# Performance work log

Hardware: AMD Instinct MI355X
Metric: run time of the kernel (lower is better)

The kernel has to match this reference:

```python
import jax, jax.numpy as jnp
import numpy as np

NUM_HEAD = 16


def setup_inputs() -> dict:
    key = jax.random.key(0)
    ks = jax.random.split(key, 4)
    B, C, D = 2, 2048, 1024
    hidden_states = jax.random.normal(ks[0], (B, C, D), dtype=jnp.float32)
    attention_mask = jnp.zeros((B, 1, C, C), dtype=jnp.float32)
    Wqkv = jax.random.normal(ks[1], (D, 3 * D), dtype=jnp.float32) * (D ** -0.5)
    bqkv = jnp.zeros((3 * D,), dtype=jnp.float32)
    Wo = jax.random.normal(ks[2], (D, D), dtype=jnp.float32) * (D ** -0.5)
    bo = jnp.zeros((D,), dtype=jnp.float32)
    return {"hidden_states": hidden_states, "attention_mask": attention_mask,
            "Wqkv": Wqkv, "bqkv": bqkv, "Wo": Wo, "bo": bo}


def reference(hidden_states, attention_mask, Wqkv, bqkv, Wo, bo):
    B, C, D = hidden_states.shape
    H = NUM_HEAD
    hd = D // H
    scaling = hd ** -0.5

    qkv = hidden_states @ Wqkv + bqkv                      # [B, C, 3D]
    q, k, v = jnp.split(qkv, 3, axis=-1)
    # [B, C, H, hd] -> [B, H, C, hd]
    q = q.reshape(B, C, H, hd).transpose(0, 2, 1, 3)
    k = k.reshape(B, C, H, hd).transpose(0, 2, 1, 3)
    v = v.reshape(B, C, H, hd).transpose(0, 2, 1, 3)

    scores = jnp.einsum("bhqd,bhkd->bhqk", q, k) * scaling  # [B, H, C, C]
    causal = jnp.tril(jnp.ones((C, C), dtype=bool))[None, None]
    mask = jnp.where(causal, attention_mask, -jnp.inf)      # [B, 1, C, C]
    probs = jax.nn.softmax(scores + mask, axis=-1)
    out = jnp.einsum("bhqk,bhkd->bhqd", probs, v)           # [B, H, C, hd]
    out = out.transpose(0, 2, 1, 3).reshape(B, C, D)
    return out @ Wo + bo
```

## Files before the change

### kernel.cpp

```cpp
#include <hip/hip_runtime.h>
#include <hip/hip_bf16.h>
#include <cstdint>
#include <cstddef>

typedef __attribute__((ext_vector_type(8))) short short8;
typedef __attribute__((ext_vector_type(4))) float f32x4;
typedef __attribute__((ext_vector_type(16))) float f32x16;
typedef unsigned short u16;
typedef unsigned int u32;

#define B_ 2
#define C_ 2048
#define D_ 1024
#define H_ 16
#define HD_ 64

static __device__ __forceinline__ u16 f2b(float f) {
  u32 x = __builtin_bit_cast(u32, f);
  x += 0x7FFFu + ((x >> 16) & 1u);
  return (u16)(x >> 16);
}
static __device__ __forceinline__ float b2f(u16 v) {
  return __builtin_bit_cast(float, (u32)v << 16);
}

static __device__ void tconv_body(const float* __restrict__ in, u16* __restrict__ out,
                                  int R, int Cc, int bx, int by, int t,
                                  float (*tile)[65]) {
  const int tC = bx * 64, tR = by * 64;
  const int r0 = t >> 4;
  const int c0 = (t & 15) * 4;
#pragma unroll
  for (int ii = 0; ii < 4; ++ii) {
    int r = ii * 16 + r0;
    float4 v = *reinterpret_cast<const float4*>(&in[(size_t)(tR + r) * Cc + tC + c0]);
    tile[r][c0] = v.x; tile[r][c0 + 1] = v.y; tile[r][c0 + 2] = v.z; tile[r][c0 + 3] = v.w;
  }
  __syncthreads();
#pragma unroll
  for (int ii = 0; ii < 4; ++ii) {
    int c = ii * 16 + r0;
    ushort4 o;
    o.x = f2b(tile[c0 + 0][c]);
    o.y = f2b(tile[c0 + 1][c]);
    o.z = f2b(tile[c0 + 2][c]);
    o.w = f2b(tile[c0 + 3][c]);
    *reinterpret_cast<ushort4*>(&out[(size_t)(tC + c) * R + tR + c0]) = o;
  }
}

__global__ __launch_bounds__(256) void k_prep(
    const float* __restrict__ hs, u16* __restrict__ hsb,
    const float* __restrict__ Wqkv, u16* __restrict__ Wqkvt,
    const float* __restrict__ Wo, u16* __restrict__ Wot,
    const float* __restrict__ mask, u32* __restrict__ flags)
{
  __shared__ float tile[64][65];
  __shared__ int sh[4];
  const int bid = blockIdx.x;
  const int t = threadIdx.x;
  if (bid < 2048) {
    int i = (bid * 256 + t) * 4;
    const int n = 4096 * 1024;
    const int stride = 2048 * 256 * 4;
    for (; i < n; i += stride) {
      float4 v = *reinterpret_cast<const float4*>(hs + i);
      ushort4 o;
      o.x = f2b(v.x); o.y = f2b(v.y); o.z = f2b(v.z); o.w = f2b(v.w);
      *reinterpret_cast<ushort4*>(hsb + i) = o;
    }
  } else if (bid < 2816) {
    const int r = bid - 2048;
    tconv_body(Wqkv, Wqkvt, 1024, 3072, r % 48, r / 48, t, tile);
  } else if (bid < 3072) {
    const int r = bid - 2816;
    tconv_body(Wo, Wot, 1024, 1024, r % 16, r / 16, t, tile);
  } else {
    const int mb = bid - 3072;
    const int kt = mb & 31, qs = (mb >> 5) & 31, b = mb >> 10;
    const float* base = mask + ((size_t)b * C_ + qs * 64) * C_ + kt * 64;
    const int row = t >> 2, c0 = (t & 3) * 16;
    int any = 0;
#pragma unroll
    for (int i = 0; i < 4; ++i) {
      float4 v = *reinterpret_cast<const float4*>(base + (size_t)row * C_ + c0 + i * 4);
      any |= (v.x != 0.f) | (v.y != 0.f) | (v.z != 0.f) | (v.w != 0.f);
    }
    const unsigned long long bal = __ballot(any);
    if ((t & 63) == 0) sh[t >> 6] = (bal != 0ull);
    __syncthreads();
    if (t == 0) flags[mb] = (u32)(sh[0] | sh[1] | sh[2] | sh[3]);
  }
}

#define GLL16(gptr, lptr) __builtin_amdgcn_global_load_lds( \
    (const __attribute__((address_space(1))) u32*)(gptr),   \
    (__attribute__((address_space(3))) u32*)(lptr), 16, 0, 0)

template<int EPI, int BM>
__global__ __launch_bounds__(256) void k_gemm(
    const u16* __restrict__ A, const u16* __restrict__ Bt,
    int M, int N, int K, const float* __restrict__ bias,
    u16* __restrict__ Cq, u16* __restrict__ Ck, u16* __restrict__ Cv,
    float* __restrict__ Cf)
{
  constexpr int WCW = (BM == 128) ? 64 : 32;
  constexpr int NF = WCW / 16;
  __shared__ __align__(16) u16 As[BM * 64];
  __shared__ __align__(16) u16 Bs[128 * 64];
  const int t = threadIdx.x;
  const int l = t & 63, w = t >> 6;
  const int wr = (BM == 128) ? (w >> 1) : 0;
  const int wc = (BM == 128) ? (w & 1) : w;
  const int lr = l & 15, lg = l >> 4;
  const int swk = lr & 7;
  const int m0 = blockIdx.y * BM, n0 = blockIdx.x * 128;
  f32x4 acc[4][NF] = {};

  for (int k0 = 0; k0 < K; k0 += 64) {
#pragma unroll
    for (int s = 0; s < BM / 32; ++s) {
      const int u = s * 256 + t;
      const int row = u >> 3, slot = (u & 7) ^ (row & 7);
      GLL16(A + (size_t)(m0 + row) * K + k0 + (slot << 3), As + (u << 3));
    }
#pragma unroll
    for (int s = 0; s < 4; ++s) {
      const int u = s * 256 + t;
      const int row = u >> 3, slot = (u & 7) ^ (row & 7);
      GLL16(Bt + (size_t)(n0 + row) * K + k0 + (slot << 3), Bs + (u << 3));
    }
    __syncthreads();
    short8 af[2][4], bfr[2][NF];
#pragma unroll
    for (int s = 0; s < 2; ++s) {
#pragma unroll
      for (int m = 0; m < 4; ++m)
        af[s][m] = *reinterpret_cast<const short8*>(
            &As[((wr * 64 + m * 16 + lr) << 6) + (((s * 4 + lg) ^ swk) << 3)]);
#pragma unroll
      for (int n = 0; n < NF; ++n)
        bfr[s][n] = *reinterpret_cast<const short8*>(
            &Bs[((wc * WCW + n * 16 + lr) << 6) + (((s * 4 + lg) ^ swk) << 3)]);
    }
#pragma unroll
    for (int s = 0; s < 2; ++s)
#pragma unroll
      for (int m = 0; m < 4; ++m)
#pragma unroll
        for (int n = 0; n < NF; ++n)
          acc[m][n] = __builtin_amdgcn_mfma_f32_16x16x32_bf16(af[s][m], bfr[s][n], acc[m][n], 0, 0, 0);
    __syncthreads();
  }

#pragma unroll
  for (int m = 0; m < 4; ++m) {
    const int mg = m0 + wr * 64 + m * 16 + lg * 4;
    const int bq = mg >> 11, c0 = mg & 2047;
#pragma unroll
    for (int n = 0; n < NF; ++n) {
      const int ng = n0 + wc * WCW + n * 16 + lr;
      const float bia = bias[ng];
      if (EPI == 0) {
        const int reg = ng >> 10, d = ng & 1023, h = d >> 6, e = d & 63;
        if (reg == 2) {
          u16* vp = Cv + (((size_t)(bq * H_ + h) * HD_ + e) << 11) + c0;
#pragma unroll
          for (int j = 0; j < 4; ++j) vp[j] = f2b(acc[m][n][j] + bia);
        } else {
          u16* dst = (reg == 0) ? Cq : Ck;
#pragma unroll
          for (int j = 0; j < 4; ++j)
            dst[(((size_t)(bq * H_ + h) * C_ + c0 + j) << 6) + e] = f2b(acc[m][n][j] + bia);
        }
      } else {
#pragma unroll
        for (int j = 0; j < 4; ++j)
          Cf[(size_t)(mg + j) * N + ng] = acc[m][n][j] + bia;
      }
    }
  }
}

static __device__ __forceinline__ void stage_kv(
    const u16* __restrict__ Kbh, const u16* __restrict__ Vbh,
    u16* Kd, u16* Vd, int kt, int t)
{
#pragma unroll
  for (int ch = 0; ch < 2; ++ch) {
    const int u = ch * 256 + t;
    const int row = u >> 3, slot = (u & 7) ^ (row & 7);
    GLL16(Kbh + (((size_t)(kt * 64 + row)) << 6) + (slot << 3), Kd + (u << 3));
    GLL16(Vbh + (((size_t)row) << 11) + kt * 64 + (slot << 3), Vd + (u << 3));
  }
}

__global__ __launch_bounds__(256) void k_attn(
    const u16* __restrict__ Q, const u16* __restrict__ Kb, const u16* __restrict__ Vt,
    const float* __restrict__ mask, const u32* __restrict__ flags,
    u16* __restrict__ O, u16* __restrict__ Opart, float2* __restrict__ ml)
{
  __shared__ __align__(16) u16 Kl[2][64 * 64];
  __shared__ __align__(16) u16 Vl[2][64 * 64];
  __shared__ __align__(16) u16 Sc[4][2304];
  const int bid = blockIdx.x;
  const int bh = bid & 31;
  const int sidx = 23 - (bid >> 5);
  int qt, seg, nseg;
  if (sidx < 8) { qt = sidx; seg = 0; nseg = 1; }
  else          { const int u = sidx - 8; qt = 8 + (u >> 1); seg = u & 1; nseg = 2; }
  const int ntiles = 2 * qt + 2;
  const int kt0 = seg * 16;
  const int kt1 = seg ? ntiles : ((ntiles < 16) ? ntiles : 16);
  const int slot = ((bh << 3) + (qt - 8)) * 2 + seg;

  const int b = bh >> 4, h = bh & 15;
  const int t = threadIdx.x;
  const int l = t & 63, w = t >> 6;
  const int q = l & 31, hi = l >> 5;
  const int q7 = q & 7;

  const u16* Kbh = Kb + (size_t)bh * (C_ * HD_);
  const u16* Vbh = Vt + (size_t)bh * (HD_ * C_);
  char* Swb = reinterpret_cast<char*>(Sc[w]);

  const int q0w = qt * 128 + w * 32;
  const int qg = q0w + q;
  const int qmaxw = q0w + 31;

  short8 aq[4];
  {
    const u16* qp = Q + ((size_t)bh * C_ + qg) * HD_ + hi * 8;
#pragma unroll
    for (int kh = 0; kh < 4; ++kh) {
      short8 v = *reinterpret_cast<const short8*>(qp + kh * 16);
#pragma unroll
      for (int i = 0; i < 8; ++i) {
        const float f = b2f((u16)v[i]) * 0.125f;
        v[i] = (short)f2b(f);
      }
      aq[kh] = v;
    }
  }

  f32x16 oa0 = {}, oa1 = {};
  float mrun = -INFINITY, srun = 0.f;
  const float* mrow = mask + ((size_t)b * C_ + qg) * C_;
  const u32* fb = flags + (size_t)(b * 32 + (q0w >> 6)) * 32;

  stage_kv(Kbh, Vbh, Kl[0], Vl[0], kt0, t);

#pragma unroll 1
  for (int kt = kt0; kt < kt1; ++kt) {
    const int cur = kt & 1;
    __syncthreads();
    if (kt + 1 < kt1) stage_kv(Kbh, Vbh, Kl[cur ^ 1], Vl[cur ^ 1], kt + 1, t);
    if (kt * 64 > qmaxw) continue;

    const char* Kc = reinterpret_cast<const char*>(Kl[cur]);
    const char* Vc = reinterpret_cast<const char*>(Vl[cur]);

    f32x16 p0 = {}, p1 = {};
#pragma unroll
    for (int kh = 0; kh < 4; ++kh) {
      const int sl = ((2 * kh + hi) ^ q7) << 4;
      const short8 k0 = *reinterpret_cast<const short8*>(Kc + q * 128 + sl);
      const short8 k1 = *reinterpret_cast<const short8*>(Kc + (32 + q) * 128 + sl);
      p0 = __builtin_amdgcn_mfma_f32_32x32x16_bf16(k0, aq[kh], p0, 0, 0, 0);
      p1 = __builtin_amdgcn_mfma_f32_32x32x16_bf16(k1, aq[kh], p1, 0, 0, 0);
    }

    if (fb[kt]) {
      const float* mp = mrow + kt * 64 + 4 * hi;
#pragma unroll
      for (int g = 0; g < 4; ++g) {
        const float4 m0 = *reinterpret_cast<const float4*>(mp + 8 * g);
        const float4 m1 = *reinterpret_cast<const float4*>(mp + 32 + 8 * g);
        p0[4*g+0] += m0.x; p0[4*g+1] += m0.y; p0[4*g+2] += m0.z; p0[4*g+3] += m0.w;
        p1[4*g+0] += m1.x; p1[4*g+1] += m1.y; p1[4*g+2] += m1.z; p1[4*g+3] += m1.w;
      }
    }
    if (kt * 64 + 63 > q0w) {
#pragma unroll
      for (int r = 0; r < 16; ++r) {
        const int kl = kt * 64 + (r & 3) + 8 * (r >> 2) + 4 * hi;
        if (kl > qg) p0[r] = -INFINITY;
        if (kl + 32 > qg) p1[r] = -INFINITY;
      }
    }

    float pm = -INFINITY;
#pragma unroll
    for (int r = 0; r < 16; ++r) pm = fmaxf(pm, fmaxf(p0[r], p1[r]));
    pm = fmaxf(pm, __shfl_xor(pm, 32));
    const float mn = fmaxf(fmaxf(mrun, pm), -1e30f);
    const float rs = __expf(mrun - mn);
    float sum = 0.f;
#pragma unroll
    for (int r = 0; r < 16; ++r) {
      p0[r] = __expf(p0[r] - mn); sum += p0[r];
      p1[r] = __expf(p1[r] - mn); sum += p1[r];
    }
    sum += __shfl_xor(sum, 32);
    srun = srun * rs + sum;
    mrun = mn;
    oa0 *= rs; oa1 *= rs;

#pragma unroll
    for (int g = 0; g < 4; ++g) {
#pragma unroll
      for (int m = 0; m < 2; ++m) {
        u32 w0, w1;
        asm("v_cvt_pk_bf16_f32 %0, %1, %2" : "=v"(w0) : "v"(p0[4*g+2*m]), "v"(p0[4*g+2*m+1]));
        asm("v_cvt_pk_bf16_f32 %0, %1, %2" : "=v"(w1) : "v"(p1[4*g+2*m]), "v"(p1[4*g+2*m+1]));
        *reinterpret_cast<u32*>(Swb + q * 128 + ((g ^ q7) << 4) + 8 * hi + 4 * m) = w0;
        *reinterpret_cast<u32*>(Swb + q * 128 + (((4 + g) ^ q7) << 4) + 8 * hi + 4 * m) = w1;
      }
    }
    asm volatile("" ::: "memory");

#pragma unroll
    for (int ks = 0; ks < 4; ++ks) {
      const int sl = ((2 * ks + hi) ^ q7) << 4;
      const short8 bp = *reinterpret_cast<const short8*>(Swb + q * 128 + sl);
      const short8 v0 = *reinterpret_cast<const short8*>(Vc + q * 128 + sl);
      const short8 v1 = *reinterpret_cast<const short8*>(Vc + (32 + q) * 128 + sl);
      oa0 = __builtin_amdgcn_mfma_f32_32x32x16_bf16(v0, bp, oa0, 0, 0, 0);
      oa1 = __builtin_amdgcn_mfma_f32_32x32x16_bf16(v1, bp, oa1, 0, 0, 0);
    }
  }

  const float rinv = 1.f / srun;
#pragma unroll
  for (int g = 0; g < 4; ++g) {
    const int d0 = 8 * g + 4 * hi;
    const float a0 = oa0[4*g+0] * rinv, a1 = oa0[4*g+1] * rinv;
    const float a2 = oa0[4*g+2] * rinv, a3 = oa0[4*g+3] * rinv;
    const float b0 = oa1[4*g+0] * rinv, b1 = oa1[4*g+1] * rinv;
    const float b2 = oa1[4*g+2] * rinv, b3 = oa1[4*g+3] * rinv;
    u32 w0, w1, w2, w3;
    asm("v_cvt_pk_bf16_f32 %0, %1, %2" : "=v"(w0) : "v"(a0), "v"(a1));
    asm("v_cvt_pk_bf16_f32 %0, %1, %2" : "=v"(w1) : "v"(a2), "v"(a3));
    asm("v_cvt_pk_bf16_f32 %0, %1, %2" : "=v"(w2) : "v"(b0), "v"(b1));
    asm("v_cvt_pk_bf16_f32 %0, %1, %2" : "=v"(w3) : "v"(b2), "v"(b3));
    *reinterpret_cast<uint2*>(Swb + q * 144 + d0 * 2) = make_uint2(w0, w1);
    *reinterpret_cast<uint2*>(Swb + q * 144 + (d0 + 32) * 2) = make_uint2(w2, w3);
  }
  asm volatile("" ::: "memory");
  const int q2 = l >> 1, hf = l & 1;
  if (nseg == 1) {
    u16* orow = O + ((size_t)b * C_ + q0w + q2) * D_ + h * 64 + hf * 32;
#pragma unroll
    for (int i = 0; i < 4; ++i) {
      const short8 v = *reinterpret_cast<const short8*>(Swb + q2 * 144 + hf * 64 + i * 16);
      *reinterpret_cast<short8*>(orow + i * 8) = v;
    }
  } else {
    u16* prow = Opart + (((size_t)slot * 128 + w * 32 + q2) << 6) + hf * 32;
#pragma unroll
    for (int i = 0; i < 4; ++i) {
      const short8 v = *reinterpret_cast<const short8*>(Swb + q2 * 144 + hf * 64 + i * 16);
      *reinterpret_cast<short8*>(prow + i * 8) = v;
    }
    if (hi == 0) ml[(size_t)slot * 128 + w * 32 + q] = make_float2(mrun, srun);
  }
}

__global__ __launch_bounds__(256) void k_merge(
    const u16* __restrict__ Opart, const float2* __restrict__ ml, u16* __restrict__ O)
{
  const int bid = blockIdx.x;
  const int bh = bid & 31;
  const int qt = 8 + (bid >> 5);
  const int slot0 = ((bh << 3) + (qt - 8)) * 2;
  const int b = bh >> 4, h = bh & 15;
  const int t = threadIdx.x;
  const int q = t >> 1, dh = t & 1;

  const float2 v0 = ml[(size_t)slot0 * 128 + q];
  const float2 v1 = ml[(size_t)(slot0 + 1) * 128 + q];
  const float M = fmaxf(v0.x, v1.x);
  const float a0 = __expf(v0.x - M) * v0.y;
  const float a1 = __expf(v1.x - M) * v1.y;
  const float rT = 1.f / (a0 + a1);
  const float r0 = a0 * rT, r1 = a1 * rT;

  const u16* p0 = Opart + (((size_t)slot0 * 128 + q) << 6) + dh * 32;
  const u16* p1 = Opart + (((size_t)(slot0 + 1) * 128 + q) << 6) + dh * 32;
  u16* orow = O + ((size_t)b * C_ + qt * 128 + q) * D_ + h * 64 + dh * 32;
#pragma unroll
  for (int i = 0; i < 4; ++i) {
    const short8 x0 = *reinterpret_cast<const short8*>(p0 + i * 8);
    const short8 x1 = *reinterpret_cast<const short8*>(p1 + i * 8);
    short8 y;
#pragma unroll
    for (int j = 0; j < 8; ++j)
      y[j] = (short)f2b(r0 * b2f((u16)x0[j]) + r1 * b2f((u16)x1[j]));
    *reinterpret_cast<short8*>(orow + i * 8) = y;
  }
}

extern "C" void kernel_launch(void* const* d_in, const int* in_sizes, int n_in,
                              void* d_out, int out_size, void* d_ws, size_t ws_size,
                              hipStream_t stream) {
  const float* hs   = (const float*)d_in[0];
  const float* mask = (const float*)d_in[1];
  const float* Wqkv = (const float*)d_in[2];
  const float* bqkv = (const float*)d_in[3];
  const float* Wo   = (const float*)d_in[4];
  const float* bo   = (const float*)d_in[5];
  float* out = (float*)d_out;
  char* ws = (char*)d_ws;

  u16*    hsb   = (u16*)(ws);
  u16*    Opart = (u16*)(ws);
  u16*    Wqkvt = (u16*)(ws + (8  << 20));
  float2* mlbuf = (float2*)(ws + (19 << 20));
  u32*    flags = (u32*)(ws + (20 << 20) + (1 << 19));
  u16*    Wot   = (u16*)(ws + (21 << 20));
  u16*    Qb    = (u16*)(ws + (24 << 20));
  u16*    Kb    = (u16*)(ws + (32 << 20));
  u16*    Vtb   = (u16*)(ws + (40 << 20));
  u16*    AOb   = (u16*)(ws + (48 << 20));

  k_prep<<<5120, 256, 0, stream>>>(hs, hsb, Wqkv, Wqkvt, Wo, Wot, mask, flags);
  k_gemm<0, 128><<<dim3(24, 32), 256, 0, stream>>>(hsb, Wqkvt, 4096, 3072, 1024, bqkv,
                                                   Qb, Kb, Vtb, nullptr);
  k_attn<<<768, 256, 0, stream>>>(Qb, Kb, Vtb, mask, flags, AOb, Opart, mlbuf);
  k_merge<<<256, 256, 0, stream>>>(Opart, mlbuf, AOb);
  k_gemm<1, 64><<<dim3(8, 64), 256, 0, stream>>>(AOb, Wot, 4096, 1024, 1024, bo,
                                                 nullptr, nullptr, nullptr, out);
}
```

Baseline: 124.4 us.

## Double-buffer GEMM LDS tiles and interleave next-tile loads with MFMA phases

Rewrites the GEMM main loop to use two LDS buffers, so the global-to-LDS loads for the next K tile are issued in chunks between four MFMA phases of the current tile. It also raises wave priority around the MFMA bursts, uses explicit waitcnt and barriers, and loads fragments per phase. The aim is to hide global load latency behind compute instead of stalling at a barrier each iteration. The cost is twice the LDS per block, which may reduce occupancy, plus more barriers per iteration.

```diff
diff --git a/kernel.cpp b/kernel.cpp
--- a/kernel.cpp
+++ b/kernel.cpp
@@ -106,8 +106,11 @@
 {
   constexpr int WCW = (BM == 128) ? 64 : 32;
   constexpr int NF = WCW / 16;
-  __shared__ __align__(16) u16 As[BM * 64];
-  __shared__ __align__(16) u16 Bs[128 * 64];
+  constexpr int AL = BM / 32;
+  constexpr int L  = AL + 4;
+  constexpr int C01 = (BM == 128) ? 3 : 2;
+  __shared__ __align__(16) u16 As[2][BM * 64];
+  __shared__ __align__(16) u16 Bs[2][128 * 64];
   const int t = threadIdx.x;
   const int l = t & 63, w = t >> 6;
   const int wr = (BM == 128) ? (w >> 1) : 0;
@@ -116,41 +119,105 @@
   const int swk = lr & 7;
   const int m0 = blockIdx.y * BM, n0 = blockIdx.x * 128;
   f32x4 acc[4][NF] = {};
-
-  for (int k0 = 0; k0 < K; k0 += 64) {
-#pragma unroll
-    for (int s = 0; s < BM / 32; ++s) {
-      const int u = s * 256 + t;
+  const int nt = K >> 6;
+
+  auto issue = [&](int Tn, int buf, int i) {
+    if (i < AL) {
+      const int u = i * 256 + t;
       const int row = u >> 3, slot = (u & 7) ^ (row & 7);
-      GLL16(A + (size_t)(m0 + row) * K + k0 + (slot << 3), As + (u << 3));
-    }
-#pragma unroll
-    for (int s = 0; s < 4; ++s) {
-      const int u = s * 256 + t;
+      GLL16(A + (size_t)(m0 + row) * K + Tn * 64 + (slot << 3), &As[buf][u << 3]);
+    } else {
+      const int u = (i - AL) * 256 + t;
       const int row = u >> 3, slot = (u & 7) ^ (row & 7);
-      GLL16(Bt + (size_t)(n0 + row) * K + k0 + (slot << 3), Bs + (u << 3));
-    }
-    __syncthreads();
-    short8 af[2][4], bfr[2][NF];
-#pragma unroll
-    for (int s = 0; s < 2; ++s) {
-#pragma unroll
-      for (int m = 0; m < 4; ++m)
-        af[s][m] = *reinterpret_cast<const short8*>(
-            &As[((wr * 64 + m * 16 + lr) << 6) + (((s * 4 + lg) ^ swk) << 3)]);
-#pragma unroll
-      for (int n = 0; n < NF; ++n)
-        bfr[s][n] = *reinterpret_cast<const short8*>(
-            &Bs[((wc * WCW + n * 16 + lr) << 6) + (((s * 4 + lg) ^ swk) << 3)]);
-    }
-#pragma unroll
-    for (int s = 0; s < 2; ++s)
-#pragma unroll
-      for (int m = 0; m < 4; ++m)
-#pragma unroll
-        for (int n = 0; n < NF; ++n)
-          acc[m][n] = __builtin_amdgcn_mfma_f32_16x16x32_bf16(af[s][m], bfr[s][n], acc[m][n], 0, 0, 0);
-    __syncthreads();
+      GLL16(Bt + (size_t)(n0 + row) * K + Tn * 64 + (slot << 3), &Bs[buf][u << 3]);
+    }
+  };
+
+#pragma unroll
+  for (int i = 0; i < L; ++i) issue(0, 0, i);
+  asm volatile("s_waitcnt vmcnt(0)" ::: "memory");
+  asm volatile("s_barrier" ::: "memory");
+
+#pragma unroll 1
+  for (int T = 0; T < nt; ++T) {
+    const int cur = T & 1, nxt = cur ^ 1;
+    const u16* Ac = As[cur];
+    const u16* Bc = Bs[cur];
+    const bool pf = (T + 1 < nt);
+    short8 bfr[NF], a0, a1;
+
+    if (pf) {
+#pragma unroll
+      for (int i = 0; i < C01; ++i) issue(T + 1, nxt, i);
+    }
+#pragma unroll
+    for (int n = 0; n < NF; ++n)
+      bfr[n] = *reinterpret_cast<const short8*>(
+          &Bc[((wc * WCW + n * 16 + lr) << 6) + ((lg ^ swk) << 3)]);
+    a0 = *reinterpret_cast<const short8*>(&Ac[((wr * 64 + lr) << 6) + ((lg ^ swk) << 3)]);
+    a1 = *reinterpret_cast<const short8*>(&Ac[((wr * 64 + 16 + lr) << 6) + ((lg ^ swk) << 3)]);
+    asm volatile("s_waitcnt lgkmcnt(0)" ::: "memory");
+    __builtin_amdgcn_sched_barrier(0);
+    __builtin_amdgcn_s_setprio(1);
+#pragma unroll
+    for (int n = 0; n < NF; ++n) {
+      acc[0][n] = __builtin_amdgcn_mfma_f32_16x16x32_bf16(a0, bfr[n], acc[0][n], 0, 0, 0);
+      acc[1][n] = __builtin_amdgcn_mfma_f32_16x16x32_bf16(a1, bfr[n], acc[1][n], 0, 0, 0);
+    }
+    __builtin_amdgcn_s_setprio(0);
+    asm volatile("s_barrier" ::: "memory");
+
+    if (pf) {
+#pragma unroll
+      for (int i = C01; i < 2 * C01; ++i) issue(T + 1, nxt, i);
+    }
+    a0 = *reinterpret_cast<const short8*>(&Ac[((wr * 64 + 32 + lr) << 6) + ((lg ^ swk) << 3)]);
+    a1 = *reinterpret_cast<const short8*>(&Ac[((wr * 64 + 48 + lr) << 6) + ((lg ^ swk) << 3)]);
+    asm volatile("s_waitcnt lgkmcnt(0)" ::: "memory");
+    __builtin_amdgcn_sched_barrier(0);
+    __builtin_amdgcn_s_setprio(1);
+#pragma unroll
+    for (int n = 0; n < NF; ++n) {
+      acc[2][n] = __builtin_amdgcn_mfma_f32_16x16x32_bf16(a0, bfr[n], acc[2][n], 0, 0, 0);
+      acc[3][n] = __builtin_amdgcn_mfma_f32_16x16x32_bf16(a1, bfr[n], acc[3][n], 0, 0, 0);
+    }
+    __builtin_amdgcn_s_setprio(0);
+    asm volatile("s_barrier" ::: "memory");
+
+    if (pf) {
+#pragma unroll
+      for (int i = 2 * C01; i < L; ++i) issue(T + 1, nxt, i);
+    }
+#pragma unroll
+    for (int n = 0; n < NF; ++n)
+      bfr[n] = *reinterpret_cast<const short8*>(
+          &Bc[((wc * WCW + n * 16 + lr) << 6) + (((4 + lg) ^ swk) << 3)]);
+    a0 = *reinterpret_cast<const short8*>(&Ac[((wr * 64 + lr) << 6) + (((4 + lg) ^ swk) << 3)]);
+    a1 = *reinterpret_cast<const short8*>(&Ac[((wr * 64 + 16 + lr) << 6) + (((4 + lg) ^ swk) << 3)]);
+    asm volatile("s_waitcnt lgkmcnt(0)" ::: "memory");
+    __builtin_amdgcn_sched_barrier(0);
+    __builtin_amdgcn_s_setprio(1);
+#pragma unroll
+    for (int n = 0; n < NF; ++n) {
+      acc[0][n] = __builtin_amdgcn_mfma_f32_16x16x32_bf16(a0, bfr[n], acc[0][n], 0, 0, 0);
+      acc[1][n] = __builtin_amdgcn_mfma_f32_16x16x32_bf16(a1, bfr[n], acc[1][n], 0, 0, 0);
+    }
+    __builtin_amdgcn_s_setprio(0);
+    asm volatile("s_barrier" ::: "memory");
+
+    a0 = *reinterpret_cast<const short8*>(&Ac[((wr * 64 + 32 + lr) << 6) + (((4 + lg) ^ swk) << 3)]);
+    a1 = *reinterpret_cast<const short8*>(&Ac[((wr * 64 + 48 + lr) << 6) + (((4 + lg) ^ swk) << 3)]);
+    asm volatile("s_waitcnt lgkmcnt(0)" ::: "memory");
+    __builtin_amdgcn_sched_barrier(0);
+    __builtin_amdgcn_s_setprio(1);
+#pragma unroll
+    for (int n = 0; n < NF; ++n) {
+      acc[2][n] = __builtin_amdgcn_mfma_f32_16x16x32_bf16(a0, bfr[n], acc[2][n], 0, 0, 0);
+      acc[3][n] = __builtin_amdgcn_mfma_f32_16x16x32_bf16(a1, bfr[n], acc[3][n], 0, 0, 0);
+    }
+    __builtin_amdgcn_s_setprio(0);
+    asm volatile("s_waitcnt vmcnt(0)" ::: "memory");
+    asm volatile("s_barrier" ::: "memory");
   }
 
 #pragma unroll
```

Result: slower. 160.2 us (+28.8%).
